# Kernel optimization log

Hardware: AMD Instinct MI355X
Metric: run time of the kernel (lower is better)

Reference implementation:

```python
import jax, jax.numpy as jnp
import numpy as np

LAMBDA_DRO = 0.1
EPSILON = 0.5
EPS = 1e-8

N, M, D, K = 2048, 4096, 512, 1000


def _cosine_matrix(a, b):
    # a: [N, d], b: [M, d] -> [N, M] cosine similarity via normalize + GEMM
    an = a / jnp.maximum(jnp.linalg.norm(a, axis=1, keepdims=True), EPS)
    bn = b / jnp.maximum(jnp.linalg.norm(b, axis=1, keepdims=True), EPS)
    return an @ bn.T


def setup_inputs() -> dict:
    key = jax.random.key(0)
    k = jax.random.split(key, 7)
    return {
        "ptr_features": jax.random.normal(k[0], (N, D), dtype=jnp.float32),
        "ptr_logits": jax.random.normal(k[1], (N, K), dtype=jnp.float32),
        "ptr_labels": jax.random.randint(k[2], (N,), 0, K),
        "nu_features": jax.random.normal(k[3], (M, D), dtype=jnp.float32),
        "nu_logits": jax.random.normal(k[4], (M, K), dtype=jnp.float32),
        "nu_labels": jax.random.randint(k[5], (M,), 0, K),
        "classifier_weights": jax.random.normal(k[6], (K, D), dtype=jnp.float32),
    }


def reference(ptr_features, ptr_logits, ptr_labels, nu_features, nu_logits,
              nu_labels, classifier_weights):
    # per-sample CE loss on nu (hard labels)
    log_probs = jax.nn.log_softmax(nu_logits, axis=1)          # [M, K]
    nu_losses = -jnp.take_along_axis(log_probs, nu_labels[:, None], axis=1)[:, 0]  # [M]

    # transport costs
    C_X = 1.0 - _cosine_matrix(ptr_features, nu_features)       # [N, M]
    ptr_emb = classifier_weights[ptr_labels]                    # [N, d]
    nu_emb = classifier_weights[nu_labels]                      # [M, d]
    C_Y = 1.0 - _cosine_matrix(ptr_emb, nu_emb)                 # [N, M]
    C_total = C_X + C_Y

    # worst-case distribution Q^lambda
    exponent = (nu_losses[None, :] - LAMBDA_DRO * C_total) / (LAMBDA_DRO * EPSILON + EPS)
    exponent = exponent - jnp.max(exponent, axis=1, keepdims=True)
    exp_terms = jnp.exp(exponent)                               # [N, M]
    weights = exp_terms / (jnp.sum(exp_terms, axis=1, keepdims=True) + EPS)
    probs = jnp.mean(weights, axis=0)                           # [M]
    probs = probs / (jnp.sum(probs) + EPS)

    dro_loss = jnp.sum(probs * nu_losses)
    total_loss = dro_loss  # semantic_loss = 0 (no moco inputs)
    return (total_loss, dro_loss, probs, jnp.mean(C_total), jnp.mean(C_X), jnp.mean(C_Y))
```

## Files before the change

kernel.cpp:

```cpp
#include <hip/hip_runtime.h>
#include <math.h>

#define N_PTR 2048
#define M_NU  4096
#define DIM   512
#define KCLS  1000
#define KPAD  1024

static constexpr float LAMBDA_ = 0.1f;
static constexpr float EPS_ = 1e-8f;
static constexpr float INV_DENOM = 1.0f / (0.1f * 0.5f + 1e-8f);

typedef short short8 __attribute__((ext_vector_type(8)));
typedef unsigned short u16x8 __attribute__((ext_vector_type(8)));
typedef float f32x4 __attribute__((ext_vector_type(4)));

__device__ __forceinline__ unsigned short f2bf(float x) {
  unsigned u = __float_as_uint(x);
  u += 0x7fff + ((u >> 16) & 1);
  return (unsigned short)(u >> 16);
}
__device__ __forceinline__ float bf2f(unsigned short h) {
  return __uint_as_float(((unsigned)h) << 16);
}

__device__ __forceinline__ void gload16(const void* g, void* l) {
  __builtin_amdgcn_global_load_lds(
      (const __attribute__((address_space(1))) unsigned int*)g,
      (__attribute__((address_space(3))) unsigned int*)l, 16, 0, 0);
}

__device__ __forceinline__ float blk_reduce_sum(float v, float* red) {
  #pragma unroll
  for (int off = 32; off > 0; off >>= 1) v += __shfl_down(v, off);
  __syncthreads();
  if ((threadIdx.x & 63) == 0) red[threadIdx.x >> 6] = v;
  __syncthreads();
  return red[0] + red[1] + red[2] + red[3];
}

__device__ __forceinline__ float blk_reduce_max(float v, float* red) {
  #pragma unroll
  for (int off = 32; off > 0; off >>= 1) v = fmaxf(v, __shfl_down(v, off));
  __syncthreads();
  if ((threadIdx.x & 63) == 0) red[threadIdx.x >> 6] = v;
  __syncthreads();
  return fmaxf(fmaxf(red[0], red[1]), fmaxf(red[2], red[3]));
}

__global__ __launch_bounds__(256) void prep_kernel(
    const float* __restrict__ ptr_f, const float* __restrict__ nu_f,
    const float* __restrict__ cls_f, const float* __restrict__ logits,
    const int* __restrict__ labels, unsigned short* __restrict__ An,
    unsigned short* __restrict__ Bn, unsigned short* __restrict__ Cn,
    float* __restrict__ losses) {
  __shared__ float red[4];
  int b = blockIdx.x;
  if (b < 1792) {
    int gid = b * 256 + threadIdx.x;
    int row = gid >> 6, lane = gid & 63;
    const float* src; unsigned short* dst; int lrow; int in_rows;
    if (row < N_PTR)             { src = ptr_f; dst = An; lrow = row;                in_rows = N_PTR; }
    else if (row < N_PTR + M_NU) { src = nu_f;  dst = Bn; lrow = row - N_PTR;        in_rows = M_NU; }
    else                         { src = cls_f; dst = Cn; lrow = row - N_PTR - M_NU; in_rows = KCLS; }
    u16x8 ov;
    if (lrow < in_rows) {
      const float4* rp = (const float4*)(src + (size_t)lrow * DIM);
      float4 a = rp[lane * 2], bq = rp[lane * 2 + 1];
      float v[8] = {a.x, a.y, a.z, a.w, bq.x, bq.y, bq.z, bq.w};
      float s = 0.f;
      #pragma unroll
      for (int j = 0; j < 8; ++j) s = fmaf(v[j], v[j], s);
      #pragma unroll
      for (int off = 32; off > 0; off >>= 1) s += __shfl_xor(s, off);
      float inv = 1.0f / fmaxf(sqrtf(s), EPS_);
      #pragma unroll
      for (int j = 0; j < 8; ++j) ov[j] = f2bf(v[j] * inv);
    } else {
      #pragma unroll
      for (int j = 0; j < 8; ++j) ov[j] = 0;
    }
    *(u16x8*)(dst + (size_t)lrow * DIM + lane * 8) = ov;
  } else {
    int row = b - 1792;
    int tid = threadIdx.x;
    const float* x = logits + (size_t)row * KCLS;
    float mx_loc = -INFINITY;
    for (int c = tid; c < KCLS; c += 256) mx_loc = fmaxf(mx_loc, x[c]);
    float mx = blk_reduce_max(mx_loc, red);
    float se_loc = 0.f;
    for (int c = tid; c < KCLS; c += 256) se_loc += expf(x[c] - mx);
    float se = blk_reduce_sum(se_loc, red);
    if (tid == 0) losses[row] = mx + logf(se) - x[labels[row]];
  }
}

template <int BM, int MODE>
__global__ __launch_bounds__(256) void mfma_gemm(
    const unsigned short* __restrict__ A, const unsigned short* __restrict__ B,
    float* __restrict__ Gf, unsigned short* __restrict__ Tb,
    const int* __restrict__ pl, const int* __restrict__ nl,
    const float* __restrict__ nu_loss, unsigned* __restrict__ gbits,
    float* __restrict__ partial_rows, float* __restrict__ s_part,
    float* __restrict__ gy_part, int ldc) {
  constexpr int FR = BM / 32;
  constexpr int WSPAN = BM / 2;
  __shared__ unsigned short Alds[BM * 64];
  __shared__ unsigned short Blds[BM * 64];
  __shared__ float red[4];
  const int tid = threadIdx.x;
  const int w = tid >> 6, lane = tid & 63;
  const int brow = blockIdx.y * BM, bcol = blockIdx.x * BM;
  const int wr = w >> 1, wc = w & 1;

  if (MODE == 0 && blockIdx.x == 0 && blockIdx.y == 0) {
    float mloc = 0.f;
    for (int i = tid; i < M_NU; i += 256) mloc = fmaxf(mloc, nu_loss[i]);
    float mx = blk_reduce_max(mloc, red);
    if (tid == 0) *gbits = __float_as_uint(mx);
    __syncthreads();
  }

  const int sr = lane >> 3;
  const int sc = lane & 7;
  const int schunk = (sc ^ sr) * 8;

  f32x4 acc[FR][FR] = {};

  for (int k0 = 0; k0 < DIM; k0 += 64) {
    #pragma unroll
    for (int i = 0; i < FR; ++i) {
      int j = w * FR + i;
      int r = j * 8 + sr;
      gload16(A + (size_t)(brow + r) * DIM + k0 + schunk, (char*)Alds + j * 1024);
      gload16(B + (size_t)(bcol + r) * DIM + k0 + schunk, (char*)Blds + j * 1024);
    }
    __syncthreads();
    #pragma unroll
    for (int kk = 0; kk < 2; ++kk) {
      const int koff = kk * 64 + (lane >> 4) * 16;
      short8 af[FR], bfr[FR];
      #pragma unroll
      for (int mi = 0; mi < FR; ++mi) {
        int r = wr * WSPAN + mi * 16 + (lane & 15);
        af[mi] = *(const short8*)((const char*)Alds + r * 128 + (koff ^ ((r & 7) << 4)));
      }
      #pragma unroll
      for (int ni = 0; ni < FR; ++ni) {
        int r = wc * WSPAN + ni * 16 + (lane & 15);
        bfr[ni] = *(const short8*)((const char*)Blds + r * 128 + (koff ^ ((r & 7) << 4)));
      }
      #pragma unroll
      for (int mi = 0; mi < FR; ++mi)
        #pragma unroll
        for (int ni = 0; ni < FR; ++ni)
          acc[mi][ni] = __builtin_amdgcn_mfma_f32_16x16x32_bf16(af[mi], bfr[ni], acc[mi][ni], 0, 0, 0);
    }
    __syncthreads();
  }

  if (MODE == 0) {
    #pragma unroll
    for (int mi = 0; mi < FR; ++mi)
      #pragma unroll
      for (int ni = 0; ni < FR; ++ni)
        #pragma unroll
        for (int j = 0; j < 4; ++j) {
          int row = brow + wr * WSPAN + mi * 16 + (lane >> 4) * 4 + j;
          int col = bcol + wc * WSPAN + ni * 16 + (lane & 15);
          Gf[(size_t)row * ldc + col] = acc[mi][ni][j];
        }
  } else {
    const float gmax = __uint_as_float(*gbits);
    const float fac = LAMBDA_ * INV_DENOM;
    int   cols[FR]; float a_r[FR]; int nl_r[FR];
    #pragma unroll
    for (int ni = 0; ni < FR; ++ni) {
      cols[ni] = bcol + wc * WSPAN + ni * 16 + (lane & 15);
      a_r[ni]  = (nu_loss[cols[ni]] - gmax - 2.f * LAMBDA_) * INV_DENOM;
      nl_r[ni] = nl[cols[ni]];
    }
    float s_acc = 0.f, gy_acc = 0.f;
    #pragma unroll
    for (int mi = 0; mi < FR; ++mi) {
      #pragma unroll
      for (int j = 0; j < 4; ++j) {
        int row = brow + wr * WSPAN + mi * 16 + (lane >> 4) * 4 + j;
        const float* Grow = Gf + (size_t)pl[row] * KPAD;
        float rowacc = 0.f;
        #pragma unroll
        for (int ni = 0; ni < FR; ++ni) {
          float s  = acc[mi][ni][j];
          float gy = Grow[nl_r[ni]];
          float e  = fmaf(fac, s + gy, a_r[ni]);
          float t  = __expf(e);
          unsigned short tb = f2bf(t);
          Tb[(size_t)row * ldc + cols[ni]] = tb;
          rowacc += bf2f(tb);
          s_acc += s; gy_acc += gy;
        }
        #pragma unroll
        for (int off = 1; off < 16; off <<= 1) rowacc += __shfl_xor(rowacc, off);
        if ((lane & 15) == 0)
          partial_rows[(size_t)(blockIdx.x * 2 + wc) * N_PTR + row] = rowacc;
      }
    }
    float stot = blk_reduce_sum(s_acc, red);
    float gtot = blk_reduce_sum(gy_acc, red);
    if (tid == 0) {
      int bid = blockIdx.y * gridDim.x + blockIdx.x;
      s_part[bid] = stot; gy_part[bid] = gtot;
    }
  }
}

__global__ __launch_bounds__(256) void colpass_kernel(
    const unsigned short* __restrict__ Tb, const float* __restrict__ partial_rows,
    float* __restrict__ partial) {
  __shared__ float winv[64];
  int m0 = blockIdx.x * 512 + threadIdx.x * 2;
  int n0 = blockIdx.y * 64;
  if (threadIdx.x < 64) {
    float rs = 0.f;
    #pragma unroll 4
    for (int cb = 0; cb < 64; ++cb) rs += partial_rows[(size_t)cb * N_PTR + n0 + threadIdx.x];
    winv[threadIdx.x] = 1.0f / (rs + EPS_);
  }
  __syncthreads();
  float a0 = 0.f, a1 = 0.f;
  #pragma unroll 4
  for (int i = 0; i < 64; ++i) {
    unsigned tv = *(const unsigned*)(Tb + (size_t)(n0 + i) * M_NU + m0);
    float wv = winv[i];
    a0 = fmaf(bf2f((unsigned short)(tv & 0xffffu)), wv, a0);
    a1 = fmaf(bf2f((unsigned short)(tv >> 16)), wv, a1);
  }
  *(float2*)(partial + (size_t)blockIdx.y * M_NU + m0) = make_float2(a0, a1);
}

__global__ __launch_bounds__(256) void f1_kernel(const float* __restrict__ partial,
    const float* __restrict__ nu_loss, float* __restrict__ out,
    float* __restrict__ T_part, float* __restrict__ D_part) {
  __shared__ float red[4];
  int m = blockIdx.x * 256 + threadIdx.x;
  float raw = 0.f;
  #pragma unroll
  for (int c = 0; c < 32; ++c) raw += partial[(size_t)c * M_NU + m];
  out[2 + m] = raw;
  float T = blk_reduce_sum(raw, red);
  float D = blk_reduce_sum(raw * nu_loss[m], red);
  if (threadIdx.x == 0) { T_part[blockIdx.x] = T; D_part[blockIdx.x] = D; }
}

__global__ __launch_bounds__(256) void f2_kernel(float* __restrict__ out,
    const float* __restrict__ T_part, const float* __restrict__ D_part,
    const float* __restrict__ s_part, const float* __restrict__ gy_part) {
  __shared__ float red[4];
  int tid = threadIdx.x;
  float lt = 0.f, ld = 0.f;
  if (tid < 16) { lt = T_part[tid]; ld = D_part[tid]; }
  float ls = 0.f, lg = 0.f;
  for (int i = tid; i < 512; i += 256) { ls += s_part[i]; lg += gy_part[i]; }
  float T  = blk_reduce_sum(lt, red);
  float D  = blk_reduce_sum(ld, red);
  float S  = blk_reduce_sum(ls, red);
  float Gy = blk_reduce_sum(lg, red);
  float scale = (1.0f / (float)N_PTR) / (T / (float)N_PTR + EPS_);
  for (int m = tid; m < M_NU; m += 256) out[2 + m] *= scale;
  if (tid == 0) {
    float dro = D * scale;
    const float invNM = 1.0f / ((float)N_PTR * (float)M_NU);
    float mcx = 1.f - S * invNM;
    float mcy = 1.f - Gy * invNM;
    out[0] = dro;
    out[1] = dro;
    out[2 + M_NU] = mcx + mcy;
    out[3 + M_NU] = mcx;
    out[4 + M_NU] = mcy;
  }
}

extern "C" void kernel_launch(void* const* d_in, const int* in_sizes, int n_in,
                              void* d_out, int out_size, void* d_ws, size_t ws_size,
                              hipStream_t stream) {
  const float* ptr_feat = (const float*)d_in[0];
  const int*   ptr_lab  = (const int*)d_in[2];
  const float* nu_feat  = (const float*)d_in[3];
  const float* nu_log   = (const float*)d_in[4];
  const int*   nu_lab   = (const int*)d_in[5];
  const float* cls_w    = (const float*)d_in[6];
  float* out = (float*)d_out;

  char* base = (char*)d_ws;
  unsigned short* Tb = (unsigned short*)base;
  float* Gf          = (float*)(base + 16u * 1024 * 1024);
  unsigned short* An = (unsigned short*)(base + 20u * 1024 * 1024);
  unsigned short* Bn = (unsigned short*)(base + 22u * 1024 * 1024);
  unsigned short* Cn = (unsigned short*)(base + 26u * 1024 * 1024);
  float* fb          = (float*)(base + 27u * 1024 * 1024);
  float* nloss        = fb;
  unsigned* gbits     = (unsigned*)(nloss + 4096);
  float* partial_rows = nloss + 4096 + 64;
  float* s_part       = partial_rows + 64 * N_PTR;
  float* gy_part      = s_part + 512;
  float* partial      = gy_part + 512;
  float* T_part       = partial + 32 * M_NU;
  float* D_part       = T_part + 16;

  prep_kernel<<<dim3(1792 + M_NU), 256, 0, stream>>>(
      ptr_feat, nu_feat, cls_w, nu_log, nu_lab, An, Bn, Cn, nloss);
  mfma_gemm<64, 0><<<dim3(KPAD / 64, KPAD / 64), 256, 0, stream>>>(
      Cn, Cn, Gf, nullptr, nullptr, nullptr, nloss, gbits,
      nullptr, nullptr, nullptr, KPAD);
  mfma_gemm<128, 1><<<dim3(M_NU / 128, N_PTR / 128), 256, 0, stream>>>(
      An, Bn, Gf, Tb, ptr_lab, nu_lab, nloss, gbits,
      partial_rows, s_part, gy_part, M_NU);
  colpass_kernel<<<dim3(M_NU / 512, N_PTR / 64), 256, 0, stream>>>(Tb, partial_rows, partial);
  f1_kernel<<<dim3(M_NU / 256), 256, 0, stream>>>(partial, nloss, out, T_part, D_part);
  f2_kernel<<<dim3(1), 256, 0, stream>>>(out, T_part, D_part, s_part, gy_part);
}
```

Baseline: 74.65 us.

## Fuse label-embedding cosine into main GEMM via K-concatenation, compute means from column sums

The main GEMM now runs over a concatenated K of 1024: the first half holds the normalized features and the second half the gathered normalized class embeddings, so C_X and C_Y similarities are summed inside the MFMA accumulation. This removes the separate 1000x1000 class GEMM, the Gf buffer and the per-element gathers in the epilogue. The means of C_X and C_Y are now computed as dot products of column sums (sum_i a_i · sum_j b_j) from a new colsum kernel. That kernel also takes over the global max of the losses. The log-softmax rows are vectorized to float4 and use fast exp. In exchange, the main GEMM does twice the K work, with gathered loads for the embedding half.

```diff
diff --git a/kernel.cpp b/kernel.cpp
--- a/kernel.cpp
+++ b/kernel.cpp
@@ -85,131 +85,143 @@
     int row = b - 1792;
     int tid = threadIdx.x;
     const float* x = logits + (size_t)row * KCLS;
+    const float4* x4 = (const float4*)x;
+    float4 v = make_float4(0.f, 0.f, 0.f, 0.f);
     float mx_loc = -INFINITY;
-    for (int c = tid; c < KCLS; c += 256) mx_loc = fmaxf(mx_loc, x[c]);
+    if (tid < 250) {
+      v = x4[tid];
+      mx_loc = fmaxf(fmaxf(v.x, v.y), fmaxf(v.z, v.w));
+    }
     float mx = blk_reduce_max(mx_loc, red);
     float se_loc = 0.f;
-    for (int c = tid; c < KCLS; c += 256) se_loc += expf(x[c] - mx);
+    if (tid < 250)
+      se_loc = __expf(v.x - mx) + __expf(v.y - mx) + __expf(v.z - mx) + __expf(v.w - mx);
     float se = blk_reduce_sum(se_loc, red);
     if (tid == 0) losses[row] = mx + logf(se) - x[labels[row]];
   }
 }
 
-template <int BM, int MODE>
+__global__ __launch_bounds__(256) void colsum_kernel(
+    const unsigned short* __restrict__ An, const unsigned short* __restrict__ Bn,
+    const unsigned short* __restrict__ Cn, const int* __restrict__ pl,
+    const int* __restrict__ nl, const float* __restrict__ nloss,
+    float* __restrict__ csum_part, unsigned* __restrict__ gbits) {
+  __shared__ float red[4];
+  int b = blockIdx.x, tid = threadIdx.x;
+  if (b == 96) {
+    float mloc = 0.f;
+    for (int i = tid; i < M_NU; i += 256) mloc = fmaxf(mloc, nloss[i]);
+    float mx = blk_reduce_max(mloc, red);
+    if (tid == 0) *gbits = __float_as_uint(mx);
+    return;
+  }
+  const unsigned short* base; const int* idx = nullptr; int n0;
+  if (b < 16)      { base = An; n0 = b * 128; }
+  else if (b < 48) { base = Bn; n0 = (b - 16) * 128; }
+  else if (b < 64) { base = Cn; idx = pl; n0 = (b - 48) * 128; }
+  else             { base = Cn; idx = nl; n0 = (b - 64) * 128; }
+  float a0 = 0.f, a1 = 0.f;
+  for (int i = 0; i < 128; ++i) {
+    int rr = n0 + i;
+    const unsigned short* rowp = base + (size_t)(idx ? idx[rr] : rr) * DIM;
+    unsigned v = *(const unsigned*)(rowp + tid * 2);
+    a0 += bf2f((unsigned short)(v & 0xffffu));
+    a1 += bf2f((unsigned short)(v >> 16));
+  }
+  csum_part[(size_t)b * DIM + tid * 2]     = a0;
+  csum_part[(size_t)b * DIM + tid * 2 + 1] = a1;
+}
+
 __global__ __launch_bounds__(256) void mfma_gemm(
-    const unsigned short* __restrict__ A, const unsigned short* __restrict__ B,
-    float* __restrict__ Gf, unsigned short* __restrict__ Tb,
-    const int* __restrict__ pl, const int* __restrict__ nl,
-    const float* __restrict__ nu_loss, unsigned* __restrict__ gbits,
-    float* __restrict__ partial_rows, float* __restrict__ s_part,
-    float* __restrict__ gy_part, int ldc) {
-  constexpr int FR = BM / 32;
-  constexpr int WSPAN = BM / 2;
-  __shared__ unsigned short Alds[BM * 64];
-  __shared__ unsigned short Blds[BM * 64];
-  __shared__ float red[4];
+    const unsigned short* __restrict__ An, const unsigned short* __restrict__ Bn,
+    const unsigned short* __restrict__ Cn, const int* __restrict__ pl,
+    const int* __restrict__ nl, const float* __restrict__ nu_loss,
+    const unsigned* __restrict__ gbits, unsigned short* __restrict__ Tb,
+    float* __restrict__ partial_rows) {
+  __shared__ unsigned short Alds[128 * 64];
+  __shared__ unsigned short Blds[128 * 64];
   const int tid = threadIdx.x;
   const int w = tid >> 6, lane = tid & 63;
-  const int brow = blockIdx.y * BM, bcol = blockIdx.x * BM;
+  const int brow = blockIdx.y * 128, bcol = blockIdx.x * 128;
   const int wr = w >> 1, wc = w & 1;
-
-  if (MODE == 0 && blockIdx.x == 0 && blockIdx.y == 0) {
-    float mloc = 0.f;
-    for (int i = tid; i < M_NU; i += 256) mloc = fmaxf(mloc, nu_loss[i]);
-    float mx = blk_reduce_max(mloc, red);
-    if (tid == 0) *gbits = __float_as_uint(mx);
-    __syncthreads();
-  }
 
   const int sr = lane >> 3;
   const int sc = lane & 7;
   const int schunk = (sc ^ sr) * 8;
 
-  f32x4 acc[FR][FR] = {};
-
-  for (int k0 = 0; k0 < DIM; k0 += 64) {
+  const unsigned short* aLo[4]; const unsigned short* aHi[4];
+  const unsigned short* bLo[4]; const unsigned short* bHi[4];
+  #pragma unroll
+  for (int i = 0; i < 4; ++i) {
+    int r = (w * 4 + i) * 8 + sr;
+    aLo[i] = An + (size_t)(brow + r) * DIM + schunk;
+    aHi[i] = Cn + (size_t)pl[brow + r] * DIM + schunk;
+    bLo[i] = Bn + (size_t)(bcol + r) * DIM + schunk;
+    bHi[i] = Cn + (size_t)nl[bcol + r] * DIM + schunk;
+  }
+
+  f32x4 acc[4][4] = {};
+
+  #pragma unroll
+  for (int kt = 0; kt < 16; ++kt) {
+    const int k0 = kt * 64;
     #pragma unroll
-    for (int i = 0; i < FR; ++i) {
-      int j = w * FR + i;
-      int r = j * 8 + sr;
-      gload16(A + (size_t)(brow + r) * DIM + k0 + schunk, (char*)Alds + j * 1024);
-      gload16(B + (size_t)(bcol + r) * DIM + k0 + schunk, (char*)Blds + j * 1024);
+    for (int i = 0; i < 4; ++i) {
+      const unsigned short* pa = (kt < 8) ? aLo[i] + k0 : aHi[i] + (k0 - DIM);
+      const unsigned short* pb = (kt < 8) ? bLo[i] + k0 : bHi[i] + (k0 - DIM);
+      gload16(pa, (char*)Alds + (w * 4 + i) * 1024);
+      gload16(pb, (char*)Blds + (w * 4 + i) * 1024);
     }
     __syncthreads();
     #pragma unroll
     for (int kk = 0; kk < 2; ++kk) {
       const int koff = kk * 64 + (lane >> 4) * 16;
-      short8 af[FR], bfr[FR];
-      #pragma unroll
-      for (int mi = 0; mi < FR; ++mi) {
-        int r = wr * WSPAN + mi * 16 + (lane & 15);
+      short8 af[4], bfr[4];
+      #pragma unroll
+      for (int mi = 0; mi < 4; ++mi) {
+        int r = wr * 64 + mi * 16 + (lane & 15);
         af[mi] = *(const short8*)((const char*)Alds + r * 128 + (koff ^ ((r & 7) << 4)));
       }
       #pragma unroll
-      for (int ni = 0; ni < FR; ++ni) {
-        int r = wc * WSPAN + ni * 16 + (lane & 15);
+      for (int ni = 0; ni < 4; ++ni) {
+        int r = wc * 64 + ni * 16 + (lane & 15);
         bfr[ni] = *(const short8*)((const char*)Blds + r * 128 + (koff ^ ((r & 7) << 4)));
       }
       #pragma unroll
-      for (int mi = 0; mi < FR; ++mi)
+      for (int mi = 0; mi < 4; ++mi)
         #pragma unroll
-        for (int ni = 0; ni < FR; ++ni)
+        for (int ni = 0; ni < 4; ++ni)
           acc[mi][ni] = __builtin_amdgcn_mfma_f32_16x16x32_bf16(af[mi], bfr[ni], acc[mi][ni], 0, 0, 0);
     }
     __syncthreads();
   }
 
-  if (MODE == 0) {
+  const float gmax = __uint_as_float(*gbits);
+  const float fac = LAMBDA_ * INV_DENOM;
+  int cols[4]; float a_r[4];
+  #pragma unroll
+  for (int ni = 0; ni < 4; ++ni) {
+    cols[ni] = bcol + wc * 64 + ni * 16 + (lane & 15);
+    a_r[ni]  = (nu_loss[cols[ni]] - gmax - 2.f * LAMBDA_) * INV_DENOM;
+  }
+  #pragma unroll
+  for (int mi = 0; mi < 4; ++mi) {
     #pragma unroll
-    for (int mi = 0; mi < FR; ++mi)
-      #pragma unroll
-      for (int ni = 0; ni < FR; ++ni)
-        #pragma unroll
-        for (int j = 0; j < 4; ++j) {
-          int row = brow + wr * WSPAN + mi * 16 + (lane >> 4) * 4 + j;
-          int col = bcol + wc * WSPAN + ni * 16 + (lane & 15);
-          Gf[(size_t)row * ldc + col] = acc[mi][ni][j];
-        }
-  } else {
-    const float gmax = __uint_as_float(*gbits);
-    const float fac = LAMBDA_ * INV_DENOM;
-    int   cols[FR]; float a_r[FR]; int nl_r[FR];
-    #pragma unroll
-    for (int ni = 0; ni < FR; ++ni) {
-      cols[ni] = bcol + wc * WSPAN + ni * 16 + (lane & 15);
-      a_r[ni]  = (nu_loss[cols[ni]] - gmax - 2.f * LAMBDA_) * INV_DENOM;
-      nl_r[ni] = nl[cols[ni]];
-    }
-    float s_acc = 0.f, gy_acc = 0.f;
-    #pragma unroll
-    for (int mi = 0; mi < FR; ++mi) {
-      #pragma unroll
-      for (int j = 0; j < 4; ++j) {
-        int row = brow + wr * WSPAN + mi * 16 + (lane >> 4) * 4 + j;
-        const float* Grow = Gf + (size_t)pl[row] * KPAD;
-        float rowacc = 0.f;
-        #pragma unroll
-        for (int ni = 0; ni < FR; ++ni) {
-          float s  = acc[mi][ni][j];
-          float gy = Grow[nl_r[ni]];
-          float e  = fmaf(fac, s + gy, a_r[ni]);
-          float t  = __expf(e);
-          unsigned short tb = f2bf(t);
-          Tb[(size_t)row * ldc + cols[ni]] = tb;
-          rowacc += bf2f(tb);
-          s_acc += s; gy_acc += gy;
-        }
-        #pragma unroll
-        for (int off = 1; off < 16; off <<= 1) rowacc += __shfl_xor(rowacc, off);
-        if ((lane & 15) == 0)
-          partial_rows[(size_t)(blockIdx.x * 2 + wc) * N_PTR + row] = rowacc;
+    for (int j = 0; j < 4; ++j) {
+      int row = brow + wr * 64 + mi * 16 + (lane >> 4) * 4 + j;
+      float rowacc = 0.f;
+      #pragma unroll
+      for (int ni = 0; ni < 4; ++ni) {
+        float e = fmaf(fac, acc[mi][ni][j], a_r[ni]);
+        float t = __expf(e);
+        unsigned short tb = f2bf(t);
+        Tb[(size_t)row * M_NU + cols[ni]] = tb;
+        rowacc += bf2f(tb);
       }
-    }
-    float stot = blk_reduce_sum(s_acc, red);
-    float gtot = blk_reduce_sum(gy_acc, red);
-    if (tid == 0) {
-      int bid = blockIdx.y * gridDim.x + blockIdx.x;
-      s_part[bid] = stot; gy_part[bid] = gtot;
+      #pragma unroll
+      for (int off = 1; off < 16; off <<= 1) rowacc += __shfl_xor(rowacc, off);
+      if ((lane & 15) == 0)
+        partial_rows[(size_t)(blockIdx.x * 2 + wc) * N_PTR + row] = rowacc;
     }
   }
 }
@@ -240,38 +252,56 @@
 
 __global__ __launch_bounds__(256) void f1_kernel(const float* __restrict__ partial,
     const float* __restrict__ nu_loss, float* __restrict__ out,
-    float* __restrict__ T_part, float* __restrict__ D_part) {
+    float* __restrict__ T_part, float* __restrict__ D_part,
+    const float* __restrict__ csum_part, float* __restrict__ PQ) {
   __shared__ float red[4];
-  int m = blockIdx.x * 256 + threadIdx.x;
-  float raw = 0.f;
-  #pragma unroll
-  for (int c = 0; c < 32; ++c) raw += partial[(size_t)c * M_NU + m];
-  out[2 + m] = raw;
-  float T = blk_reduce_sum(raw, red);
-  float D = blk_reduce_sum(raw * nu_loss[m], red);
-  if (threadIdx.x == 0) { T_part[blockIdx.x] = T; D_part[blockIdx.x] = D; }
+  int b = blockIdx.x, tid = threadIdx.x;
+  if (b < 16) {
+    int m = b * 256 + tid;
+    float raw = 0.f;
+    #pragma unroll
+    for (int c = 0; c < 32; ++c) raw += partial[(size_t)c * M_NU + m];
+    out[2 + m] = raw;
+    float T = blk_reduce_sum(raw, red);
+    float D = blk_reduce_sum(raw * nu_loss[m], red);
+    if (tid == 0) { T_part[b] = T; D_part[b] = D; }
+  } else {
+    int j = b - 16;
+    const int starts[4] = {0, 16, 48, 64};
+    const int cnts[4]   = {16, 32, 16, 32};
+    float a0 = 0.f, a1 = 0.f;
+    for (int p = 0; p < cnts[j]; ++p) {
+      const float* cp = csum_part + (size_t)(starts[j] + p) * DIM;
+      a0 += cp[tid * 2]; a1 += cp[tid * 2 + 1];
+    }
+    PQ[(size_t)j * DIM + tid * 2]     = a0;
+    PQ[(size_t)j * DIM + tid * 2 + 1] = a1;
+  }
 }
 
 __global__ __launch_bounds__(256) void f2_kernel(float* __restrict__ out,
     const float* __restrict__ T_part, const float* __restrict__ D_part,
-    const float* __restrict__ s_part, const float* __restrict__ gy_part) {
+    const float* __restrict__ PQ, const float* __restrict__ nu_loss) {
   __shared__ float red[4];
   int tid = threadIdx.x;
   float lt = 0.f, ld = 0.f;
   if (tid < 16) { lt = T_part[tid]; ld = D_part[tid]; }
-  float ls = 0.f, lg = 0.f;
-  for (int i = tid; i < 512; i += 256) { ls += s_part[i]; lg += gy_part[i]; }
+  float lx = 0.f, ly = 0.f;
+  for (int c = tid; c < DIM; c += 256) {
+    lx = fmaf(PQ[c], PQ[DIM + c], lx);
+    ly = fmaf(PQ[2 * DIM + c], PQ[3 * DIM + c], ly);
+  }
   float T  = blk_reduce_sum(lt, red);
   float D  = blk_reduce_sum(ld, red);
-  float S  = blk_reduce_sum(ls, red);
-  float Gy = blk_reduce_sum(lg, red);
+  float dX = blk_reduce_sum(lx, red);
+  float dY = blk_reduce_sum(ly, red);
   float scale = (1.0f / (float)N_PTR) / (T / (float)N_PTR + EPS_);
   for (int m = tid; m < M_NU; m += 256) out[2 + m] *= scale;
   if (tid == 0) {
     float dro = D * scale;
     const float invNM = 1.0f / ((float)N_PTR * (float)M_NU);
-    float mcx = 1.f - S * invNM;
-    float mcy = 1.f - Gy * invNM;
+    float mcx = 1.f - dX * invNM;
+    float mcy = 1.f - dY * invNM;
     out[0] = dro;
     out[1] = dro;
     out[2 + M_NU] = mcx + mcy;
@@ -293,29 +323,26 @@
 
   char* base = (char*)d_ws;
   unsigned short* Tb = (unsigned short*)base;
-  float* Gf          = (float*)(base + 16u * 1024 * 1024);
-  unsigned short* An = (unsigned short*)(base + 20u * 1024 * 1024);
-  unsigned short* Bn = (unsigned short*)(base + 22u * 1024 * 1024);
-  unsigned short* Cn = (unsigned short*)(base + 26u * 1024 * 1024);
-  float* fb          = (float*)(base + 27u * 1024 * 1024);
+  unsigned short* An = (unsigned short*)(base + 16u * 1024 * 1024);
+  unsigned short* Bn = (unsigned short*)(base + 18u * 1024 * 1024);
+  unsigned short* Cn = (unsigned short*)(base + 22u * 1024 * 1024);
+  float* fb          = (float*)(base + 23u * 1024 * 1024);
   float* nloss        = fb;
   unsigned* gbits     = (unsigned*)(nloss + 4096);
   float* partial_rows = nloss + 4096 + 64;
-  float* s_part       = partial_rows + 64 * N_PTR;
-  float* gy_part      = s_part + 512;
-  float* partial      = gy_part + 512;
+  float* partial      = partial_rows + 64 * N_PTR;
   float* T_part       = partial + 32 * M_NU;
   float* D_part       = T_part + 16;
+  float* csum_part    = D_part + 48;
+  float* PQ           = csum_part + 96 * DIM;
 
   prep_kernel<<<dim3(1792 + M_NU), 256, 0, stream>>>(
       ptr_feat, nu_feat, cls_w, nu_log, nu_lab, An, Bn, Cn, nloss);
-  mfma_gemm<64, 0><<<dim3(KPAD / 64, KPAD / 64), 256, 0, stream>>>(
-      Cn, Cn, Gf, nullptr, nullptr, nullptr, nloss, gbits,
-      nullptr, nullptr, nullptr, KPAD);
-  mfma_gemm<128, 1><<<dim3(M_NU / 128, N_PTR / 128), 256, 0, stream>>>(
-      An, Bn, Gf, Tb, ptr_lab, nu_lab, nloss, gbits,
-      partial_rows, s_part, gy_part, M_NU);
+  colsum_kernel<<<dim3(97), 256, 0, stream>>>(
+      An, Bn, Cn, ptr_lab, nu_lab, nloss, csum_part, gbits);
+  mfma_gemm<<<dim3(M_NU / 128, N_PTR / 128), 256, 0, stream>>>(
+      An, Bn, Cn, ptr_lab, nu_lab, nloss, gbits, Tb, partial_rows);
   colpass_kernel<<<dim3(M_NU / 512, N_PTR / 64), 256, 0, stream>>>(Tb, partial_rows, partial);
-  f1_kernel<<<dim3(M_NU / 256), 256, 0, stream>>>(partial, nloss, out, T_part, D_part);
-  f2_kernel<<<dim3(1), 256, 0, stream>>>(out, T_part, D_part, s_part, gy_part);
-}
+  f1_kernel<<<dim3(20), 256, 0, stream>>>(partial, nloss, out, T_part, D_part, csum_part, PQ);
+  f2_kernel<<<dim3(1), 256, 0, stream>>>(out, T_part, D_part, PQ, nloss);
+}
```

Result: slower. 77.37 us (+3.6%).

## Fuse tail reductions, store label Gram in bf16, vectorize CE logits

Applied to the files above, without the earlier changes.

The label-embedding Gram matrix is now stored as bf16, which halves its gather traffic in the main GEMM epilogue. The epilogue also accumulates per-row loss-weighted sums, so T and D can be computed row-wise inside a merged colpass kernel. That kernel and a single final kernel replace the three tail kernels, removing one launch and the serial single-block scaling pass. The cross-entropy prep now uses one float4 load per thread and fast exp. The trade-off is reduced precision in the C_Y term and its mean, plus an extra partial buffer written and read.

```diff
diff --git a/kernel.cpp b/kernel.cpp
--- a/kernel.cpp
+++ b/kernel.cpp
@@ -85,11 +85,17 @@
     int row = b - 1792;
     int tid = threadIdx.x;
     const float* x = logits + (size_t)row * KCLS;
+    const float4* x4 = (const float4*)x;
+    float4 v = make_float4(0.f, 0.f, 0.f, 0.f);
     float mx_loc = -INFINITY;
-    for (int c = tid; c < KCLS; c += 256) mx_loc = fmaxf(mx_loc, x[c]);
+    if (tid < 250) {
+      v = x4[tid];
+      mx_loc = fmaxf(fmaxf(v.x, v.y), fmaxf(v.z, v.w));
+    }
     float mx = blk_reduce_max(mx_loc, red);
     float se_loc = 0.f;
-    for (int c = tid; c < KCLS; c += 256) se_loc += expf(x[c] - mx);
+    if (tid < 250)
+      se_loc = __expf(v.x - mx) + __expf(v.y - mx) + __expf(v.z - mx) + __expf(v.w - mx);
     float se = blk_reduce_sum(se_loc, red);
     if (tid == 0) losses[row] = mx + logf(se) - x[labels[row]];
   }
@@ -98,11 +104,11 @@
 template <int BM, int MODE>
 __global__ __launch_bounds__(256) void mfma_gemm(
     const unsigned short* __restrict__ A, const unsigned short* __restrict__ B,
-    float* __restrict__ Gf, unsigned short* __restrict__ Tb,
+    unsigned short* __restrict__ Gfb, unsigned short* __restrict__ Tb,
     const int* __restrict__ pl, const int* __restrict__ nl,
     const float* __restrict__ nu_loss, unsigned* __restrict__ gbits,
-    float* __restrict__ partial_rows, float* __restrict__ s_part,
-    float* __restrict__ gy_part, int ldc) {
+    float* __restrict__ pr, float* __restrict__ pr2,
+    float* __restrict__ s_part, float* __restrict__ gy_part, int ldc) {
   constexpr int FR = BM / 32;
   constexpr int WSPAN = BM / 2;
   __shared__ unsigned short Alds[BM * 64];
@@ -168,17 +174,18 @@
         for (int j = 0; j < 4; ++j) {
           int row = brow + wr * WSPAN + mi * 16 + (lane >> 4) * 4 + j;
           int col = bcol + wc * WSPAN + ni * 16 + (lane & 15);
-          Gf[(size_t)row * ldc + col] = acc[mi][ni][j];
+          Gfb[(size_t)row * ldc + col] = f2bf(acc[mi][ni][j]);
         }
   } else {
     const float gmax = __uint_as_float(*gbits);
     const float fac = LAMBDA_ * INV_DENOM;
-    int   cols[FR]; float a_r[FR]; int nl_r[FR];
+    int cols[FR]; float a_r[FR]; float loss_r[FR]; int nl_r[FR];
     #pragma unroll
     for (int ni = 0; ni < FR; ++ni) {
-      cols[ni] = bcol + wc * WSPAN + ni * 16 + (lane & 15);
-      a_r[ni]  = (nu_loss[cols[ni]] - gmax - 2.f * LAMBDA_) * INV_DENOM;
-      nl_r[ni] = nl[cols[ni]];
+      cols[ni]  = bcol + wc * WSPAN + ni * 16 + (lane & 15);
+      loss_r[ni] = nu_loss[cols[ni]];
+      a_r[ni]   = (loss_r[ni] - gmax - 2.f * LAMBDA_) * INV_DENOM;
+      nl_r[ni]  = nl[cols[ni]];
     }
     float s_acc = 0.f, gy_acc = 0.f;
     #pragma unroll
@@ -186,23 +193,30 @@
       #pragma unroll
       for (int j = 0; j < 4; ++j) {
         int row = brow + wr * WSPAN + mi * 16 + (lane >> 4) * 4 + j;
-        const float* Grow = Gf + (size_t)pl[row] * KPAD;
-        float rowacc = 0.f;
+        const unsigned short* Grow = Gfb + (size_t)pl[row] * KPAD;
+        float rowacc = 0.f, rowacc2 = 0.f;
         #pragma unroll
         for (int ni = 0; ni < FR; ++ni) {
           float s  = acc[mi][ni][j];
-          float gy = Grow[nl_r[ni]];
+          float gy = bf2f(Grow[nl_r[ni]]);
           float e  = fmaf(fac, s + gy, a_r[ni]);
           float t  = __expf(e);
           unsigned short tb = f2bf(t);
           Tb[(size_t)row * ldc + cols[ni]] = tb;
-          rowacc += bf2f(tb);
+          float tt = bf2f(tb);
+          rowacc  += tt;
+          rowacc2 += tt * loss_r[ni];
           s_acc += s; gy_acc += gy;
         }
         #pragma unroll
-        for (int off = 1; off < 16; off <<= 1) rowacc += __shfl_xor(rowacc, off);
-        if ((lane & 15) == 0)
-          partial_rows[(size_t)(blockIdx.x * 2 + wc) * N_PTR + row] = rowacc;
+        for (int off = 1; off < 16; off <<= 1) {
+          rowacc  += __shfl_xor(rowacc, off);
+          rowacc2 += __shfl_xor(rowacc2, off);
+        }
+        if ((lane & 15) == 0) {
+          pr [(size_t)(blockIdx.x * 2 + wc) * N_PTR + row] = rowacc;
+          pr2[(size_t)(blockIdx.x * 2 + wc) * N_PTR + row] = rowacc2;
+        }
       }
     }
     float stot = blk_reduce_sum(s_acc, red);
@@ -214,69 +228,92 @@
   }
 }
 
-__global__ __launch_bounds__(256) void colpass_kernel(
-    const unsigned short* __restrict__ Tb, const float* __restrict__ partial_rows,
-    float* __restrict__ partial) {
-  __shared__ float winv[64];
-  int m0 = blockIdx.x * 512 + threadIdx.x * 2;
-  int n0 = blockIdx.y * 64;
-  if (threadIdx.x < 64) {
-    float rs = 0.f;
+__global__ __launch_bounds__(256) void colpass_td_kernel(
+    const unsigned short* __restrict__ Tb, const float* __restrict__ pr,
+    const float* __restrict__ pr2, float* __restrict__ partial,
+    float* __restrict__ T_part, float* __restrict__ D_part) {
+  __shared__ float sh[64];
+  int b = blockIdx.x, tid = threadIdx.x;
+  if (b < 256) {
+    int bx = b & 7, by = b >> 3;
+    int m0 = bx * 512 + tid * 2;
+    int n0 = by * 64;
+    if (tid < 64) {
+      float rs = 0.f;
+      #pragma unroll 4
+      for (int cb = 0; cb < 64; ++cb) rs += pr[(size_t)cb * N_PTR + n0 + tid];
+      sh[tid] = 1.0f / (rs + EPS_);
+    }
+    __syncthreads();
+    float a0 = 0.f, a1 = 0.f;
     #pragma unroll 4
-    for (int cb = 0; cb < 64; ++cb) rs += partial_rows[(size_t)cb * N_PTR + n0 + threadIdx.x];
-    winv[threadIdx.x] = 1.0f / (rs + EPS_);
-  }
-  __syncthreads();
-  float a0 = 0.f, a1 = 0.f;
-  #pragma unroll 4
-  for (int i = 0; i < 64; ++i) {
-    unsigned tv = *(const unsigned*)(Tb + (size_t)(n0 + i) * M_NU + m0);
-    float wv = winv[i];
-    a0 = fmaf(bf2f((unsigned short)(tv & 0xffffu)), wv, a0);
-    a1 = fmaf(bf2f((unsigned short)(tv >> 16)), wv, a1);
-  }
-  *(float2*)(partial + (size_t)blockIdx.y * M_NU + m0) = make_float2(a0, a1);
-}
-
-__global__ __launch_bounds__(256) void f1_kernel(const float* __restrict__ partial,
-    const float* __restrict__ nu_loss, float* __restrict__ out,
-    float* __restrict__ T_part, float* __restrict__ D_part) {
+    for (int i = 0; i < 64; ++i) {
+      unsigned tv = *(const unsigned*)(Tb + (size_t)(n0 + i) * M_NU + m0);
+      float wv = sh[i];
+      a0 = fmaf(bf2f((unsigned short)(tv & 0xffffu)), wv, a0);
+      a1 = fmaf(bf2f((unsigned short)(tv >> 16)), wv, a1);
+    }
+    *(float2*)(partial + (size_t)by * M_NU + m0) = make_float2(a0, a1);
+  } else {
+    int n = (b - 256) * 128 + (tid & 127);
+    float tl = 0.f, dl = 0.f;
+    if (tid < 128) {
+      float rs = 0.f, wl = 0.f;
+      #pragma unroll 4
+      for (int cb = 0; cb < 64; ++cb) {
+        rs += pr [(size_t)cb * N_PTR + n];
+        wl += pr2[(size_t)cb * N_PTR + n];
+      }
+      float wi = 1.0f / (rs + EPS_);
+      tl = rs * wi; dl = wl * wi;
+    }
+    __syncthreads();
+    #pragma unroll
+    for (int off = 32; off > 0; off >>= 1) { tl += __shfl_down(tl, off); dl += __shfl_down(dl, off); }
+    if ((tid & 63) == 0) { sh[tid >> 6] = tl; sh[4 + (tid >> 6)] = dl; }
+    __syncthreads();
+    if (tid == 0) {
+      T_part[b - 256] = sh[0] + sh[1] + sh[2] + sh[3];
+      D_part[b - 256] = sh[4] + sh[5] + sh[6] + sh[7];
+    }
+  }
+}
+
+__global__ __launch_bounds__(256) void final_kernel(const float* __restrict__ partial,
+    const float* __restrict__ T_part, const float* __restrict__ D_part,
+    const float* __restrict__ s_part, const float* __restrict__ gy_part,
+    float* __restrict__ out) {
   __shared__ float red[4];
-  int m = blockIdx.x * 256 + threadIdx.x;
-  float raw = 0.f;
+  int b = blockIdx.x, tid = threadIdx.x;
+  float T = 0.f;
   #pragma unroll
-  for (int c = 0; c < 32; ++c) raw += partial[(size_t)c * M_NU + m];
-  out[2 + m] = raw;
-  float T = blk_reduce_sum(raw, red);
-  float D = blk_reduce_sum(raw * nu_loss[m], red);
-  if (threadIdx.x == 0) { T_part[blockIdx.x] = T; D_part[blockIdx.x] = D; }
-}
-
-__global__ __launch_bounds__(256) void f2_kernel(float* __restrict__ out,
-    const float* __restrict__ T_part, const float* __restrict__ D_part,
-    const float* __restrict__ s_part, const float* __restrict__ gy_part) {
-  __shared__ float red[4];
-  int tid = threadIdx.x;
-  float lt = 0.f, ld = 0.f;
-  if (tid < 16) { lt = T_part[tid]; ld = D_part[tid]; }
-  float ls = 0.f, lg = 0.f;
-  for (int i = tid; i < 512; i += 256) { ls += s_part[i]; lg += gy_part[i]; }
-  float T  = blk_reduce_sum(lt, red);
-  float D  = blk_reduce_sum(ld, red);
-  float S  = blk_reduce_sum(ls, red);
-  float Gy = blk_reduce_sum(lg, red);
+  for (int i = 0; i < 16; ++i) T += T_part[i];
   float scale = (1.0f / (float)N_PTR) / (T / (float)N_PTR + EPS_);
-  for (int m = tid; m < M_NU; m += 256) out[2 + m] *= scale;
-  if (tid == 0) {
-    float dro = D * scale;
-    const float invNM = 1.0f / ((float)N_PTR * (float)M_NU);
-    float mcx = 1.f - S * invNM;
-    float mcy = 1.f - Gy * invNM;
-    out[0] = dro;
-    out[1] = dro;
-    out[2 + M_NU] = mcx + mcy;
-    out[3 + M_NU] = mcx;
-    out[4 + M_NU] = mcy;
+  if (b < 16) {
+    int m = b * 256 + tid;
+    float raw = 0.f;
+    #pragma unroll
+    for (int c = 0; c < 32; ++c) raw += partial[(size_t)c * M_NU + m];
+    out[2 + m] = raw * scale;
+  } else {
+    float D = 0.f;
+    #pragma unroll
+    for (int i = 0; i < 16; ++i) D += D_part[i];
+    float ls = 0.f, lg = 0.f;
+    for (int i = tid; i < 512; i += 256) { ls += s_part[i]; lg += gy_part[i]; }
+    float S  = blk_reduce_sum(ls, red);
+    float Gy = blk_reduce_sum(lg, red);
+    if (tid == 0) {
+      float dro = D * scale;
+      const float invNM = 1.0f / ((float)N_PTR * (float)M_NU);
+      float mcx = 1.f - S * invNM;
+      float mcy = 1.f - Gy * invNM;
+      out[0] = dro;
+      out[1] = dro;
+      out[2 + M_NU] = mcx + mcy;
+      out[3 + M_NU] = mcx;
+      out[4 + M_NU] = mcy;
+    }
   }
 }
 
@@ -292,30 +329,30 @@
   float* out = (float*)d_out;
 
   char* base = (char*)d_ws;
-  unsigned short* Tb = (unsigned short*)base;
-  float* Gf          = (float*)(base + 16u * 1024 * 1024);
-  unsigned short* An = (unsigned short*)(base + 20u * 1024 * 1024);
-  unsigned short* Bn = (unsigned short*)(base + 22u * 1024 * 1024);
-  unsigned short* Cn = (unsigned short*)(base + 26u * 1024 * 1024);
-  float* fb          = (float*)(base + 27u * 1024 * 1024);
-  float* nloss        = fb;
-  unsigned* gbits     = (unsigned*)(nloss + 4096);
-  float* partial_rows = nloss + 4096 + 64;
-  float* s_part       = partial_rows + 64 * N_PTR;
-  float* gy_part      = s_part + 512;
-  float* partial      = gy_part + 512;
-  float* T_part       = partial + 32 * M_NU;
-  float* D_part       = T_part + 16;
+  unsigned short* Tb  = (unsigned short*)base;
+  unsigned short* Gfb = (unsigned short*)(base + 16u * 1024 * 1024);
+  unsigned short* An  = (unsigned short*)(base + 18u * 1024 * 1024);
+  unsigned short* Bn  = (unsigned short*)(base + 20u * 1024 * 1024);
+  unsigned short* Cn  = (unsigned short*)(base + 24u * 1024 * 1024);
+  float* fb           = (float*)(base + 25u * 1024 * 1024);
+  float* nloss   = fb;
+  unsigned* gbits= (unsigned*)(nloss + 4096);
+  float* pr      = nloss + 4096 + 64;
+  float* pr2     = pr  + 64 * N_PTR;
+  float* partial = pr2 + 64 * N_PTR;
+  float* s_part  = partial + 32 * M_NU;
+  float* gy_part = s_part + 512;
+  float* T_part  = gy_part + 512;
+  float* D_part  = T_part + 16;
 
   prep_kernel<<<dim3(1792 + M_NU), 256, 0, stream>>>(
       ptr_feat, nu_feat, cls_w, nu_log, nu_lab, An, Bn, Cn, nloss);
   mfma_gemm<64, 0><<<dim3(KPAD / 64, KPAD / 64), 256, 0, stream>>>(
-      Cn, Cn, Gf, nullptr, nullptr, nullptr, nloss, gbits,
-      nullptr, nullptr, nullptr, KPAD);
+      Cn, Cn, Gfb, nullptr, nullptr, nullptr, nloss, gbits,
+      nullptr, nullptr, nullptr, nullptr, KPAD);
   mfma_gemm<128, 1><<<dim3(M_NU / 128, N_PTR / 128), 256, 0, stream>>>(
-      An, Bn, Gf, Tb, ptr_lab, nu_lab, nloss, gbits,
-      partial_rows, s_part, gy_part, M_NU);
-  colpass_kernel<<<dim3(M_NU / 512, N_PTR / 64), 256, 0, stream>>>(Tb, partial_rows, partial);
-  f1_kernel<<<dim3(M_NU / 256), 256, 0, stream>>>(partial, nloss, out, T_part, D_part);
-  f2_kernel<<<dim3(1), 256, 0, stream>>>(out, T_part, D_part, s_part, gy_part);
-}
+      An, Bn, Gfb, Tb, ptr_lab, nu_lab, nloss, gbits,
+      pr, pr2, s_part, gy_part, M_NU);
+  colpass_td_kernel<<<dim3(272), 256, 0, stream>>>(Tb, pr, pr2, partial, T_part, D_part);
+  final_kernel<<<dim3(17), 256, 0, stream>>>(partial, T_part, D_part, s_part, gy_part, out);
+}
```

New measurement: 62.79 us, median of 2. 1.19x faster.
